# Kernel optimization log

Hardware: AMD Instinct MI355X
Metric: run time of the kernel (lower is better)

## Reference

```python
import jax, jax.numpy as jnp
import numpy as np

B, T, N, D, E, H = 4, 512, 512, 1024, 1024, 16
HD = D // H
EPS = 1e-6

def _ln(h):
    mu = jnp.mean(h, axis=-1, keepdims=True)
    var = jnp.mean(jnp.square(h - mu), axis=-1, keepdims=True)
    return (h - mu) / jnp.sqrt(var + EPS)

def setup_inputs() -> dict:
    key = jax.random.key(0)
    ks = jax.random.split(key, 20)
    s = 0.02
    return {
        "x1": jax.random.normal(ks[0], (B, T, D), jnp.float32),
        "x2": jax.random.normal(ks[1], (B, T, D), jnp.float32),
        "x3": jax.random.normal(ks[2], (B, T, D), jnp.float32),
        "xf": jax.random.normal(ks[3], (B, N, D), jnp.float32),
        "emb": jax.random.normal(ks[4], (B, E), jnp.float32),
        "key_padding_mask": jnp.zeros((B, N), dtype=bool),
        # AdaLN params (branch-stacked), weights stored (in,out)
        "adaln_w": jax.random.normal(ks[5], (3, E, 2 * D), jnp.float32) * s,
        "adaln_b": jnp.zeros((3, 2 * D), jnp.float32),
        "xf_adaln_w": jax.random.normal(ks[6], (E, 2 * D), jnp.float32) * s,
        "xf_adaln_b": jnp.zeros((2 * D,), jnp.float32),
        "q_w": jax.random.normal(ks[7], (3, D, D), jnp.float32) * s,
        "q_b": jnp.zeros((3, D), jnp.float32),
        "k_w": jax.random.normal(ks[8], (D, D), jnp.float32) * s,
        "k_b": jnp.zeros((D,), jnp.float32),
        "v_w": jax.random.normal(ks[9], (D, D), jnp.float32) * s,
        "v_b": jnp.zeros((D,), jnp.float32),
        "out_w": jax.random.normal(ks[10], (3, D, D), jnp.float32) * s,
        "out_b": jnp.zeros((3, D), jnp.float32),
    }

def reference(x1, x2, x3, xf, emb, key_padding_mask,
              adaln_w, adaln_b, xf_adaln_w, xf_adaln_b,
              q_w, q_b, k_w, k_b, v_w, v_b, out_w, out_b):
    se = jax.nn.silu(emb)  # (B,E)
    xs = [x1, x2, x3]
    Qs = []
    for i in range(3):
        eo = se @ adaln_w[i] + adaln_b[i]            # (B,2D)
        scale, shift = jnp.split(eo, 2, axis=-1)
        h = _ln(xs[i]) * (1.0 + scale[:, None]) + shift[:, None]
        Qs.append((h @ q_w[i] + q_b[i]).reshape(B, T, H, HD))
    Q = jnp.concatenate(Qs, axis=1)                  # (B,3T,H,HD)

    eo = se @ xf_adaln_w + xf_adaln_b
    scale, shift = jnp.split(eo, 2, axis=-1)
    xfn = _ln(xf) * (1.0 + scale[:, None]) + shift[:, None]
    K = (xfn @ k_w + k_b).reshape(B, N, H, HD)
    V = (xfn @ v_w + v_b).reshape(B, N, H, HD)

    logits = jnp.einsum('bthd,bnhd->bhtn', Q, K) / jnp.sqrt(jnp.float32(HD))
    logits = jnp.where(key_padding_mask[:, None, None, :], -jnp.inf, logits)
    attn = jax.nn.softmax(logits, axis=-1)           # dropout is identity (eval)
    out = jnp.einsum('bhtn,bnhd->bthd', attn, V).reshape(B, 3 * T, D)

    out1 = out[:, :T] @ out_w[0] + out_b[0]
    out2 = out[:, T:2 * T] @ out_w[1] + out_b[1]
    out3 = out[:, 2 * T:3 * T] @ out_w[2] + out_b[2]
    return (out1, out2, out3)
```

## Files before the change

### kernel.cpp

```cpp
#include <hip/hip_runtime.h>
#include <hip/hip_bf16.h>
#include <stdint.h>

#define BB 4
#define TSEQ 512
#define NSEQ 512
#define DD 1024
#define EE 1024
#define HH 16
#define HD 64

typedef __attribute__((ext_vector_type(8))) short bf16x8;
typedef __attribute__((ext_vector_type(4))) float f32x4;

__device__ __forceinline__ unsigned short f2bf(float f) {
    union { float f; uint32_t u; } v; v.f = f;
    uint32_t u = v.u;
    uint32_t r = (u + 0x7fffu + ((u >> 16) & 1u)) >> 16;
    return (unsigned short)r;
}

__device__ __forceinline__ uint32_t pkbf(float a, float b) {
    __hip_bfloat162 t = __float22bfloat162_rn(float2{a, b});
    return *(uint32_t*)&t;
}

#define GLD16(gp, lp)                                                          \
    __builtin_amdgcn_global_load_lds(                                          \
        (const __attribute__((address_space(1))) unsigned int*)(gp),           \
        (__attribute__((address_space(3))) unsigned int*)(lp), 16, 0, 0)

__global__ __launch_bounds__(256) void tw_all_kernel(
    const float* __restrict__ q_w, const float* __restrict__ k_w,
    const float* __restrict__ v_w, const float* __restrict__ out_w,
    unsigned short* __restrict__ qwt, unsigned short* __restrict__ kwt,
    unsigned short* __restrict__ vwt, unsigned short* __restrict__ owt)
{
    __shared__ __align__(16) unsigned short Ts[64 * 72];
    int k0 = blockIdx.x * 64, n0 = blockIdx.y * 64;
    int z = blockIdx.z;
    const float* in; unsigned short* out;
    if (z < 3)       { in = q_w + (size_t)z * DD * DD;         out = qwt + (size_t)z * DD * DD; }
    else if (z == 3) { in = k_w;                               out = kwt; }
    else if (z == 4) { in = v_w;                               out = vwt; }
    else             { in = out_w + (size_t)(z - 5) * DD * DD; out = owt + (size_t)(z - 5) * DD * DD; }
    int tid = threadIdx.x;
    int r = tid >> 2, c0 = (tid & 3) * 16;
#pragma unroll
    for (int i = 0; i < 4; i++) {
        float4 v = *(const float4*)(in + (size_t)(k0 + r) * DD + n0 + c0 + i * 4);
        Ts[(c0 + i * 4 + 0) * 72 + r] = f2bf(v.x);
        Ts[(c0 + i * 4 + 1) * 72 + r] = f2bf(v.y);
        Ts[(c0 + i * 4 + 2) * 72 + r] = f2bf(v.z);
        Ts[(c0 + i * 4 + 3) * 72 + r] = f2bf(v.w);
    }
    __syncthreads();
#pragma unroll
    for (int i = 0; i < 2; i++) {
        int idx = i * 256 + tid;
        int row = idx >> 3, ko = (idx & 7) * 8;
        *(uint4*)(out + (size_t)(n0 + row) * DD + k0 + ko) =
            *(const uint4*)(Ts + row * 72 + ko);
    }
}

__global__ __launch_bounds__(256) void adaln_kernel(
    const float* __restrict__ emb,
    const float* __restrict__ adaln_w, const float* __restrict__ adaln_b,
    const float* __restrict__ xf_w, const float* __restrict__ xf_b,
    float* __restrict__ scaleB, float* __restrict__ shiftB)
{
    __shared__ __align__(16) float seT[EE][4];
    __shared__ float buf[128 * 33];
    int tid = threadIdx.x;
    int chunk = blockIdx.x, j = blockIdx.y;
#pragma unroll
    for (int b = 0; b < 4; b++) {
        float4 e4 = ((const float4*)(emb + (size_t)b * EE))[tid];
        seT[tid * 4 + 0][b] = e4.x / (1.f + __expf(-e4.x));
        seT[tid * 4 + 1][b] = e4.y / (1.f + __expf(-e4.y));
        seT[tid * 4 + 2][b] = e4.z / (1.f + __expf(-e4.z));
        seT[tid * 4 + 3][b] = e4.w / (1.f + __expf(-e4.w));
    }
    __syncthreads();
    const float* W    = (j < 3) ? (adaln_w + (size_t)j * EE * 2 * DD) : xf_w;
    const float* bias = (j < 3) ? (adaln_b + (size_t)j * 2 * DD) : xf_b;
    int eg = tid >> 3, cg = tid & 7;
    int c0 = chunk * 32 + cg * 4;
    const float* Wp = W + (size_t)(eg * 32) * (2 * DD) + c0;
    float4 a0 = {0,0,0,0}, a1 = {0,0,0,0}, a2 = {0,0,0,0}, a3 = {0,0,0,0};
#pragma unroll 8
    for (int e = 0; e < 32; e++) {
        float4 w = *(const float4*)(Wp + (size_t)e * (2 * DD));
        float4 s = *(const float4*)&seT[eg * 32 + e][0];
        a0.x += s.x * w.x; a0.y += s.x * w.y; a0.z += s.x * w.z; a0.w += s.x * w.w;
        a1.x += s.y * w.x; a1.y += s.y * w.y; a1.z += s.y * w.z; a1.w += s.y * w.w;
        a2.x += s.z * w.x; a2.y += s.z * w.y; a2.z += s.z * w.z; a2.w += s.z * w.w;
        a3.x += s.w * w.x; a3.y += s.w * w.y; a3.z += s.w * w.z; a3.w += s.w * w.w;
    }
    float accs[4][4] = {{a0.x,a0.y,a0.z,a0.w},{a1.x,a1.y,a1.z,a1.w},
                        {a2.x,a2.y,a2.z,a2.w},{a3.x,a3.y,a3.z,a3.w}};
#pragma unroll
    for (int b = 0; b < 4; b++)
#pragma unroll
        for (int i = 0; i < 4; i++)
            buf[(b * 32 + cg * 4 + i) * 33 + eg] = accs[b][i];
    __syncthreads();
    if (tid < 128) {
        int b = tid >> 5, cl = tid & 31;
        float s = 0.f;
#pragma unroll 8
        for (int e = 0; e < 32; e++) s += buf[(b * 32 + cl) * 33 + e];
        int c = chunk * 32 + cl;
        float v = s + bias[c];
        if (c < DD) scaleB[(size_t)(j * 4 + b) * DD + c] = v;
        else        shiftB[(size_t)(j * 4 + b) * DD + (c - DD)] = v;
    }
}

__global__ __launch_bounds__(256) void ln_mod_kernel(
    const float* __restrict__ x1, const float* __restrict__ x2,
    const float* __restrict__ x3, const float* __restrict__ xf,
    const float* __restrict__ scaleB, const float* __restrict__ shiftB,
    unsigned short* __restrict__ hq, unsigned short* __restrict__ hx)
{
    __shared__ float rs[4], rq[4];
    int row = blockIdx.x, tid = threadIdx.x;
    const float* src; unsigned short* dst; int sb;
    if (row < 6144) {
        int b = row / 1536, t3 = row % 1536;
        int br = t3 >> 9, t = t3 & 511;
        const float* xs = (br == 0) ? x1 : ((br == 1) ? x2 : x3);
        src = xs + ((size_t)b * TSEQ + t) * DD;
        dst = hq + (size_t)row * DD;
        sb = br * 4 + b;
    } else {
        int idx = row - 6144;
        src = xf + (size_t)idx * DD;
        dst = hx + (size_t)idx * DD;
        sb = 12 + (idx >> 9);
    }
    float4 x = ((const float4*)src)[tid];
    float s = x.x + x.y + x.z + x.w;
    float q = x.x * x.x + x.y * x.y + x.z * x.z + x.w * x.w;
    for (int o = 1; o < 64; o <<= 1) { s += __shfl_xor(s, o, 64); q += __shfl_xor(q, o, 64); }
    int lane = tid & 63, wid = tid >> 6;
    if (lane == 0) { rs[wid] = s; rq[wid] = q; }
    __syncthreads();
    float S = rs[0] + rs[1] + rs[2] + rs[3];
    float Q = rq[0] + rq[1] + rq[2] + rq[3];
    float mu = S * (1.f / DD);
    float var = Q * (1.f / DD) - mu * mu;
    float rstd = rsqrtf(var + 1e-6f);
    float4 sc = ((const float4*)(scaleB + (size_t)sb * DD))[tid];
    float4 sh = ((const float4*)(shiftB + (size_t)sb * DD))[tid];
    ushort4 o;
    o.x = f2bf((x.x - mu) * rstd * (1.f + sc.x) + sh.x);
    o.y = f2bf((x.y - mu) * rstd * (1.f + sc.y) + sh.y);
    o.z = f2bf((x.z - mu) * rstd * (1.f + sc.z) + sh.z);
    o.w = f2bf((x.w - mu) * rstd * (1.f + sc.w) + sh.w);
    ((ushort4*)dst)[tid] = o;
}

__device__ __forceinline__ void gemm_core64x128(
    const unsigned short* __restrict__ A, const unsigned short* __restrict__ W,
    int m0, int n0, unsigned short* As, unsigned short* Bs,
    int tid, f32x4 acc[2][4])
{
    int lane = tid & 63, wid = tid >> 6;
    int fm = lane & 15, quad = lane >> 4;
    int wm = wid >> 1, wn = wid & 1;
    int sr = tid >> 3;
    int sc = tid & 7;
    int gko = (sc ^ (sr & 7)) * 8;
    const unsigned short* Ap = A + (size_t)(m0 + sr) * DD + gko;
    const unsigned short* Wp = W + (size_t)(n0 + sr) * DD + gko;
    unsigned short* la = As + tid * 8;
    unsigned short* lb = Bs + tid * 8;
    int f7 = fm & 7;
    for (int k0 = 0; k0 < DD; k0 += 64) {
#pragma unroll
        for (int i = 0; i < 2; i++)
            GLD16(Ap + (size_t)(32 * i) * DD + k0, la + i * 2048);
#pragma unroll
        for (int i = 0; i < 4; i++)
            GLD16(Wp + (size_t)(32 * i) * DD + k0, lb + i * 2048);
        __syncthreads();
#pragma unroll
        for (int kh = 0; kh < 2; kh++) {
            int sq = ((quad + 4 * kh) ^ f7) * 8;
            bf16x8 af[2], bfr[4];
#pragma unroll
            for (int mt = 0; mt < 2; mt++)
                af[mt] = *(const bf16x8*)(As + (wm * 32 + mt * 16 + fm) * 64 + sq);
#pragma unroll
            for (int nt = 0; nt < 4; nt++)
                bfr[nt] = *(const bf16x8*)(Bs + (wn * 64 + nt * 16 + fm) * 64 + sq);
#pragma unroll
            for (int mt = 0; mt < 2; mt++)
#pragma unroll
                for (int nt = 0; nt < 4; nt++)
                    acc[mt][nt] = __builtin_amdgcn_mfma_f32_16x16x32_bf16(af[mt], bfr[nt], acc[mt][nt], 0, 0, 0);
        }
        __syncthreads();
    }
}

__global__ __launch_bounds__(256) void q_gemm(
    const unsigned short* __restrict__ hq, const unsigned short* __restrict__ qwt,
    const float* __restrict__ q_b, unsigned short* __restrict__ Qpk)
{
    __shared__ __align__(16) unsigned short As[64 * 64];
    __shared__ __align__(16) unsigned short Bs[128 * 64];
    int id = blockIdx.x;
    int ty = id % 96, n0 = (id / 96) * 128;
    int m0 = ty * 64;
    int br = (m0 % 1536) >> 9;
    const unsigned short* W = qwt + (size_t)br * DD * DD;
    const float* bias = q_b + (size_t)br * DD;
    int tid = threadIdx.x, lane = tid & 63, wid = tid >> 6;
    int fm = lane & 15, quad = lane >> 4;
    int wm = wid >> 1, wn = wid & 1;
    f32x4 z = {0.f, 0.f, 0.f, 0.f};
    f32x4 acc[2][4];
#pragma unroll
    for (int mt = 0; mt < 2; mt++)
#pragma unroll
        for (int nt = 0; nt < 4; nt++) acc[mt][nt] = z;
    gemm_core64x128(hq, W, m0, n0, As, Bs, tid, acc);
#pragma unroll
    for (int mt = 0; mt < 2; mt++) {
#pragma unroll
        for (int nt = 0; nt < 4; nt++) {
            int c = n0 + wn * 64 + nt * 16 + fm;
            float bv = bias[c];
            int r0 = m0 + wm * 32 + mt * 16 + quad * 4;
            int h = c >> 6;
            int b = r0 / 1536, t3 = r0 % 1536;
            int kk = (c >> 5) & 1, o = c & 31;
            size_t base = ((((size_t)(b * HH + h) * 2 + kk) * 1536) + t3) * 32 + o;
#pragma unroll
            for (int reg = 0; reg < 4; reg++)
                Qpk[base + (size_t)reg * 32] = f2bf((acc[mt][nt][reg] + bv) * 0.125f);
        }
    }
}

__global__ __launch_bounds__(256) void kv_gemm(
    const unsigned short* __restrict__ hx,
    const unsigned short* __restrict__ kwt, const unsigned short* __restrict__ vwt,
    const float* __restrict__ k_b, const float* __restrict__ v_b,
    unsigned short* __restrict__ Kpk, unsigned short* __restrict__ Vpk)
{
    __shared__ __align__(16) unsigned short As[64 * 64];
    __shared__ __align__(16) unsigned short Bs[128 * 64];
    int id = blockIdx.x;
    int ty = id % 64, n0 = (id / 64) * 128;
    int isV = ty >> 5;
    int m0 = (ty & 31) * 64;
    const unsigned short* W = isV ? vwt : kwt;
    const float* bias = isV ? v_b : k_b;
    int tid = threadIdx.x, lane = tid & 63, wid = tid >> 6;
    int fm = lane & 15, quad = lane >> 4;
    int wm = wid >> 1, wn = wid & 1;
    f32x4 z = {0.f, 0.f, 0.f, 0.f};
    f32x4 acc[2][4];
#pragma unroll
    for (int mt = 0; mt < 2; mt++)
#pragma unroll
        for (int nt = 0; nt < 4; nt++) acc[mt][nt] = z;
    gemm_core64x128(hx, W, m0, n0, As, Bs, tid, acc);
#pragma unroll
    for (int mt = 0; mt < 2; mt++) {
#pragma unroll
        for (int nt = 0; nt < 4; nt++) {
            int c = n0 + wn * 64 + nt * 16 + fm;
            float bv = bias[c];
            int r0 = m0 + wm * 32 + mt * 16 + quad * 4;
            int h = c >> 6;
            int b = r0 >> 9, n = r0 & 511;
            if (!isV) {
                int kk = (c >> 5) & 1, o = c & 31;
                size_t base = ((((size_t)(b * HH + h) * 2 + kk) * 512) + n) * 32 + o;
#pragma unroll
                for (int reg = 0; reg < 4; reg++)
                    Kpk[base + (size_t)reg * 32] = f2bf(acc[mt][nt][reg] + bv);
            } else {
                int hd = c & 63, cv = n >> 5, ko = n & 31;
                ushort4 st;
                st.x = f2bf(acc[mt][nt][0] + bv);
                st.y = f2bf(acc[mt][nt][1] + bv);
                st.z = f2bf(acc[mt][nt][2] + bv);
                st.w = f2bf(acc[mt][nt][3] + bv);
                *(ushort4*)(Vpk + ((((size_t)(b * HH + h) * 16 + cv) * 64) + hd) * 32 + ko) = st;
            }
        }
    }
}

__global__ __launch_bounds__(256) void out_gemm(
    const unsigned short* __restrict__ Ain, const unsigned short* __restrict__ owt,
    const float* __restrict__ out_b, float* __restrict__ outp)
{
    __shared__ __align__(16) unsigned short As[64 * 64];
    __shared__ __align__(16) unsigned short Bs[128 * 64];
    int id = blockIdx.x;
    int ty = id % 96, n0 = (id / 96) * 128;
    int m0 = ty * 64;
    int br = (m0 % 1536) >> 9;
    const unsigned short* W = owt + (size_t)br * DD * DD;
    const float* bias = out_b + (size_t)br * DD;
    int tid = threadIdx.x, lane = tid & 63, wid = tid >> 6;
    int fm = lane & 15, quad = lane >> 4;
    int wm = wid >> 1, wn = wid & 1;
    f32x4 z = {0.f, 0.f, 0.f, 0.f};
    f32x4 acc[2][4];
#pragma unroll
    for (int mt = 0; mt < 2; mt++)
#pragma unroll
        for (int nt = 0; nt < 4; nt++) acc[mt][nt] = z;
    gemm_core64x128(Ain, W, m0, n0, As, Bs, tid, acc);
#pragma unroll
    for (int mt = 0; mt < 2; mt++) {
#pragma unroll
        for (int nt = 0; nt < 4; nt++) {
            int c = n0 + wn * 64 + nt * 16 + fm;
            float bv = bias[c];
            int r0 = m0 + wm * 32 + mt * 16 + quad * 4;
            int b = r0 / 1536, t3 = r0 % 1536, t = t3 & 511;
#pragma unroll
            for (int reg = 0; reg < 4; reg++)
                outp[(size_t)br * (BB * TSEQ * DD) + (size_t)b * (TSEQ * DD)
                     + (size_t)(t + reg) * DD + c] = acc[mt][nt][reg] + bv;
        }
    }
}

__global__ __launch_bounds__(256, 4) void attn_kernel(
    const unsigned short* __restrict__ Qpk,
    const unsigned short* __restrict__ Kpk,
    const unsigned short* __restrict__ Vpk,
    const unsigned char* __restrict__ mask,
    unsigned short* __restrict__ attn)
{
    __shared__ __align__(16) unsigned short P[32 * 520];
    __shared__ float redsum[128];
    int orig = blockIdx.x;
    int wg = (orig & 7) * 384 + (orig >> 3);
    int bh = wg / 48, b = bh >> 4, h = bh & 15;
    int m0 = (wg % 48) * 32;
    int tid = threadIdx.x, lane = tid & 63, w = tid >> 6;
    int fm = lane & 15, quad = lane >> 4;

    const unsigned char* mp = mask + (size_t)b * NSEQ + w * 128;
    unsigned long long mw0 = __ballot(mp[lane] != 0);
    unsigned long long mw1 = __ballot(mp[64 + lane] != 0);

    f32x4 acc[8][2];
#pragma unroll
    for (int mt = 0; mt < 8; mt++) {
        unsigned long long word = (mt >= 4) ? mw1 : mw0;
        int kb = (mt * 16 + quad * 4) & 63;
        f32x4 ini;
#pragma unroll
        for (int reg = 0; reg < 4; reg++)
            ini[reg] = ((word >> (kb + reg)) & 1ull) ? -1e30f : 0.f;
        acc[mt][0] = ini; acc[mt][1] = ini;
    }
    const unsigned short* Kbase = Kpk + (size_t)bh * 2 * 512 * 32 + quad * 8;
    const unsigned short* Qbase = Qpk + (size_t)bh * 2 * 1536 * 32 + quad * 8;
    const unsigned short* Vbase = Vpk + (size_t)bh * 16 * 64 * 32 + (size_t)(w * 16 + fm) * 32 + quad * 8;
#pragma unroll
    for (int kk = 0; kk < 2; kk++) {
        bf16x8 bq0 = *(const bf16x8*)(Qbase + (size_t)(kk * 1536 + m0 + fm) * 32);
        bf16x8 bq1 = *(const bf16x8*)(Qbase + (size_t)(kk * 1536 + m0 + 16 + fm) * 32);
#pragma unroll
        for (int mt = 0; mt < 8; mt++) {
            bf16x8 ak = *(const bf16x8*)(Kbase + (size_t)(kk * 512 + w * 128 + mt * 16 + fm) * 32);
            acc[mt][0] = __builtin_amdgcn_mfma_f32_16x16x32_bf16(ak, bq0, acc[mt][0], 0, 0, 0);
            acc[mt][1] = __builtin_amdgcn_mfma_f32_16x16x32_bf16(ak, bq1, acc[mt][1], 0, 0, 0);
        }
    }

    bf16x8 vpre[8];
#pragma unroll
    for (int kk = 0; kk < 8; kk++)
        vpre[kk] = *(const bf16x8*)(Vbase + (size_t)kk * 64 * 32);

    float s0 = 0.f, s1 = 0.f;
#pragma unroll
    for (int mt = 0; mt < 8; mt++) {
        float e00 = __expf(acc[mt][0][0]);
        float e01 = __expf(acc[mt][0][1]);
        float e02 = __expf(acc[mt][0][2]);
        float e03 = __expf(acc[mt][0][3]);
        float e10 = __expf(acc[mt][1][0]);
        float e11 = __expf(acc[mt][1][1]);
        float e12 = __expf(acc[mt][1][2]);
        float e13 = __expf(acc[mt][1][3]);
        s0 += (e00 + e01) + (e02 + e03);
        s1 += (e10 + e11) + (e12 + e13);
        uint2 p0, p1;
        p0.x = pkbf(e00, e01); p0.y = pkbf(e02, e03);
        p1.x = pkbf(e10, e11); p1.y = pkbf(e12, e13);
        int kb = w * 128 + mt * 16 + quad * 4;
        *(uint2*)(P + (size_t)fm * 520 + kb) = p0;
        *(uint2*)(P + (size_t)(16 + fm) * 520 + kb) = p1;
    }
    s0 += __shfl_xor(s0, 16, 64); s0 += __shfl_xor(s0, 32, 64);
    s1 += __shfl_xor(s1, 16, 64); s1 += __shfl_xor(s1, 32, 64);
    if (quad == 0) { redsum[w * 32 + fm] = s0; redsum[w * 32 + 16 + fm] = s1; }
    __syncthreads();

    float inv0 = 1.f / (redsum[fm] + redsum[32 + fm] + redsum[64 + fm] + redsum[96 + fm]);
    float inv1 = 1.f / (redsum[16 + fm] + redsum[48 + fm] + redsum[80 + fm] + redsum[112 + fm]);
    bf16x8 vrest[8];
#pragma unroll
    for (int kk = 0; kk < 8; kk++)
        vrest[kk] = *(const bf16x8*)(Vbase + (size_t)(8 + kk) * 64 * 32);
    f32x4 z = {0.f, 0.f, 0.f, 0.f};
    f32x4 o0 = z, o1 = z;
    const unsigned short* Pp0 = P + (size_t)fm * 520 + quad * 8;
    const unsigned short* Pp1 = P + (size_t)(16 + fm) * 520 + quad * 8;
#pragma unroll
    for (int kk = 0; kk < 8; kk++) {
        bf16x8 p0 = *(const bf16x8*)(Pp0 + kk * 32);
        bf16x8 p1 = *(const bf16x8*)(Pp1 + kk * 32);
        o0 = __builtin_amdgcn_mfma_f32_16x16x32_bf16(vpre[kk], p0, o0, 0, 0, 0);
        o1 = __builtin_amdgcn_mfma_f32_16x16x32_bf16(vpre[kk], p1, o1, 0, 0, 0);
    }
#pragma unroll
    for (int kk = 0; kk < 8; kk++) {
        bf16x8 p0 = *(const bf16x8*)(Pp0 + (8 + kk) * 32);
        bf16x8 p1 = *(const bf16x8*)(Pp1 + (8 + kk) * 32);
        o0 = __builtin_amdgcn_mfma_f32_16x16x32_bf16(vrest[kk], p0, o0, 0, 0, 0);
        o1 = __builtin_amdgcn_mfma_f32_16x16x32_bf16(vrest[kk], p1, o1, 0, 0, 0);
    }
    ushort4 r0, r1;
    r0.x = f2bf(o0[0] * inv0); r0.y = f2bf(o0[1] * inv0);
    r0.z = f2bf(o0[2] * inv0); r0.w = f2bf(o0[3] * inv0);
    r1.x = f2bf(o1[0] * inv1); r1.y = f2bf(o1[1] * inv1);
    r1.z = f2bf(o1[2] * inv1); r1.w = f2bf(o1[3] * inv1);
    *(ushort4*)(attn + ((size_t)(b * 1536 + m0 + fm)) * DD + h * HD + w * 16 + quad * 4) = r0;
    *(ushort4*)(attn + ((size_t)(b * 1536 + m0 + 16 + fm)) * DD + h * HD + w * 16 + quad * 4) = r1;
}

extern "C" void kernel_launch(void* const* d_in, const int* in_sizes, int n_in,
                              void* d_out, int out_size, void* d_ws, size_t ws_size,
                              hipStream_t stream)
{
    const float* x1   = (const float*)d_in[0];
    const float* x2   = (const float*)d_in[1];
    const float* x3   = (const float*)d_in[2];
    const float* xf   = (const float*)d_in[3];
    const float* emb  = (const float*)d_in[4];
    const unsigned char* mask = (const unsigned char*)d_in[5];
    const float* adaln_w = (const float*)d_in[6];
    const float* adaln_b = (const float*)d_in[7];
    const float* xf_w = (const float*)d_in[8];
    const float* xf_b = (const float*)d_in[9];
    const float* q_w  = (const float*)d_in[10];
    const float* q_b  = (const float*)d_in[11];
    const float* k_w  = (const float*)d_in[12];
    const float* k_b  = (const float*)d_in[13];
    const float* v_w  = (const float*)d_in[14];
    const float* v_b  = (const float*)d_in[15];
    const float* out_w = (const float*)d_in[16];
    const float* out_b = (const float*)d_in[17];

    char* ws = (char*)d_ws;
    float* scaleB        = (float*)(ws + 0);
    float* shiftB        = (float*)(ws + 65536);
    unsigned short* hq   = (unsigned short*)(ws + 131072);
    unsigned short* hx   = (unsigned short*)(ws + 12713984);
    unsigned short* Qpk  = (unsigned short*)(ws + 16908288);
    unsigned short* Kpk  = (unsigned short*)(ws + 29491200);
    unsigned short* Vpk  = (unsigned short*)(ws + 33685504);
    unsigned short* qwt  = (unsigned short*)(ws + 37879808);
    unsigned short* kwt  = (unsigned short*)(ws + 44171264);
    unsigned short* vwt  = (unsigned short*)(ws + 46268416);
    unsigned short* owt  = (unsigned short*)(ws + 48365568);

    tw_all_kernel<<<dim3(16, 16, 8), 256, 0, stream>>>(q_w, k_w, v_w, out_w,
                                                       qwt, kwt, vwt, owt);
    adaln_kernel<<<dim3(64, 4), 256, 0, stream>>>(emb, adaln_w, adaln_b, xf_w, xf_b,
                                                  scaleB, shiftB);
    ln_mod_kernel<<<8192, 256, 0, stream>>>(x1, x2, x3, xf, scaleB, shiftB, hq, hx);
    kv_gemm<<<512, 256, 0, stream>>>(hx, kwt, vwt, k_b, v_b, Kpk, Vpk);
    q_gemm<<<768, 256, 0, stream>>>(hq, qwt, q_b, Qpk);
    attn_kernel<<<3072, 256, 0, stream>>>(Qpk, Kpk, Vpk, mask, hq);
    out_gemm<<<768, 256, 0, stream>>>(hq, owt, out_b, (float*)d_out);
}
```

Measured before the change: 260.5 us.

## Halve attention query tile to 16 rows and double grid for occupancy

The attention kernel now processes 16 query rows per workgroup instead of 32. Grid size doubles to 6144 and the launch bound rises to 6 waves per SIMD. V fragments are no longer prefetched into registers but loaded inline in the PV loop, which cuts register and LDS use. The trade-off is that each K and V tile is reused by half as many query rows, so K/V traffic doubles, and the PV loop loses its prefetch overlap.

```diff
diff --git a/kernel.cpp b/kernel.cpp
--- a/kernel.cpp
+++ b/kernel.cpp
@@ -336,19 +336,19 @@
     }
 }
 
-__global__ __launch_bounds__(256, 4) void attn_kernel(
+__global__ __launch_bounds__(256, 6) void attn_kernel(
     const unsigned short* __restrict__ Qpk,
     const unsigned short* __restrict__ Kpk,
     const unsigned short* __restrict__ Vpk,
     const unsigned char* __restrict__ mask,
     unsigned short* __restrict__ attn)
 {
-    __shared__ __align__(16) unsigned short P[32 * 520];
-    __shared__ float redsum[128];
+    __shared__ __align__(16) unsigned short P[16 * 520];
+    __shared__ float redsum[64];
     int orig = blockIdx.x;
-    int wg = (orig & 7) * 384 + (orig >> 3);
-    int bh = wg / 48, b = bh >> 4, h = bh & 15;
-    int m0 = (wg % 48) * 32;
+    int wg = (orig & 7) * 768 + (orig >> 3);
+    int bh = wg / 96, b = bh >> 4, h = bh & 15;
+    int m0 = (wg % 96) * 16;
     int tid = threadIdx.x, lane = tid & 63, w = tid >> 6;
     int fm = lane & 15, quad = lane >> 4;
 
@@ -356,7 +356,7 @@
     unsigned long long mw0 = __ballot(mp[lane] != 0);
     unsigned long long mw1 = __ballot(mp[64 + lane] != 0);
 
-    f32x4 acc[8][2];
+    f32x4 acc[8];
 #pragma unroll
     for (int mt = 0; mt < 8; mt++) {
         unsigned long long word = (mt >= 4) ? mw1 : mw0;
@@ -365,84 +365,52 @@
 #pragma unroll
         for (int reg = 0; reg < 4; reg++)
             ini[reg] = ((word >> (kb + reg)) & 1ull) ? -1e30f : 0.f;
-        acc[mt][0] = ini; acc[mt][1] = ini;
+        acc[mt] = ini;
     }
     const unsigned short* Kbase = Kpk + (size_t)bh * 2 * 512 * 32 + quad * 8;
     const unsigned short* Qbase = Qpk + (size_t)bh * 2 * 1536 * 32 + quad * 8;
     const unsigned short* Vbase = Vpk + (size_t)bh * 16 * 64 * 32 + (size_t)(w * 16 + fm) * 32 + quad * 8;
 #pragma unroll
     for (int kk = 0; kk < 2; kk++) {
-        bf16x8 bq0 = *(const bf16x8*)(Qbase + (size_t)(kk * 1536 + m0 + fm) * 32);
-        bf16x8 bq1 = *(const bf16x8*)(Qbase + (size_t)(kk * 1536 + m0 + 16 + fm) * 32);
+        bf16x8 bq = *(const bf16x8*)(Qbase + (size_t)(kk * 1536 + m0 + fm) * 32);
 #pragma unroll
         for (int mt = 0; mt < 8; mt++) {
             bf16x8 ak = *(const bf16x8*)(Kbase + (size_t)(kk * 512 + w * 128 + mt * 16 + fm) * 32);
-            acc[mt][0] = __builtin_amdgcn_mfma_f32_16x16x32_bf16(ak, bq0, acc[mt][0], 0, 0, 0);
-            acc[mt][1] = __builtin_amdgcn_mfma_f32_16x16x32_bf16(ak, bq1, acc[mt][1], 0, 0, 0);
+            acc[mt] = __builtin_amdgcn_mfma_f32_16x16x32_bf16(ak, bq, acc[mt], 0, 0, 0);
         }
     }
 
-    bf16x8 vpre[8];
-#pragma unroll
-    for (int kk = 0; kk < 8; kk++)
-        vpre[kk] = *(const bf16x8*)(Vbase + (size_t)kk * 64 * 32);
-
-    float s0 = 0.f, s1 = 0.f;
+    float s0 = 0.f;
 #pragma unroll
     for (int mt = 0; mt < 8; mt++) {
-        float e00 = __expf(acc[mt][0][0]);
-        float e01 = __expf(acc[mt][0][1]);
-        float e02 = __expf(acc[mt][0][2]);
-        float e03 = __expf(acc[mt][0][3]);
-        float e10 = __expf(acc[mt][1][0]);
-        float e11 = __expf(acc[mt][1][1]);
-        float e12 = __expf(acc[mt][1][2]);
-        float e13 = __expf(acc[mt][1][3]);
-        s0 += (e00 + e01) + (e02 + e03);
-        s1 += (e10 + e11) + (e12 + e13);
-        uint2 p0, p1;
-        p0.x = pkbf(e00, e01); p0.y = pkbf(e02, e03);
-        p1.x = pkbf(e10, e11); p1.y = pkbf(e12, e13);
+        float e0 = __expf(acc[mt][0]);
+        float e1 = __expf(acc[mt][1]);
+        float e2 = __expf(acc[mt][2]);
+        float e3 = __expf(acc[mt][3]);
+        s0 += (e0 + e1) + (e2 + e3);
+        uint2 p;
+        p.x = pkbf(e0, e1); p.y = pkbf(e2, e3);
         int kb = w * 128 + mt * 16 + quad * 4;
-        *(uint2*)(P + (size_t)fm * 520 + kb) = p0;
-        *(uint2*)(P + (size_t)(16 + fm) * 520 + kb) = p1;
-    }
-    s0 += __shfl_xor(s0, 16, 64); s0 += __shfl_xor(s0, 32, 64);
-    s1 += __shfl_xor(s1, 16, 64); s1 += __shfl_xor(s1, 32, 64);
-    if (quad == 0) { redsum[w * 32 + fm] = s0; redsum[w * 32 + 16 + fm] = s1; }
+        *(uint2*)(P + (size_t)fm * 520 + kb) = p;
+    }
+    s0 += __shfl_xor(s0, 16, 64);
+    s0 += __shfl_xor(s0, 32, 64);
+    if (quad == 0) redsum[w * 16 + fm] = s0;
     __syncthreads();
 
-    float inv0 = 1.f / (redsum[fm] + redsum[32 + fm] + redsum[64 + fm] + redsum[96 + fm]);
-    float inv1 = 1.f / (redsum[16 + fm] + redsum[48 + fm] + redsum[80 + fm] + redsum[112 + fm]);
-    bf16x8 vrest[8];
-#pragma unroll
-    for (int kk = 0; kk < 8; kk++)
-        vrest[kk] = *(const bf16x8*)(Vbase + (size_t)(8 + kk) * 64 * 32);
-    f32x4 z = {0.f, 0.f, 0.f, 0.f};
-    f32x4 o0 = z, o1 = z;
+    float inv0 = 1.f / (redsum[fm] + redsum[16 + fm] + redsum[32 + fm] + redsum[48 + fm]);
+    f32x4 o0 = {0.f, 0.f, 0.f, 0.f};
     const unsigned short* Pp0 = P + (size_t)fm * 520 + quad * 8;
-    const unsigned short* Pp1 = P + (size_t)(16 + fm) * 520 + quad * 8;
-#pragma unroll
-    for (int kk = 0; kk < 8; kk++) {
+#pragma unroll
+    for (int kk = 0; kk < 16; kk++) {
+        bf16x8 av = *(const bf16x8*)(Vbase + (size_t)kk * 64 * 32);
         bf16x8 p0 = *(const bf16x8*)(Pp0 + kk * 32);
-        bf16x8 p1 = *(const bf16x8*)(Pp1 + kk * 32);
-        o0 = __builtin_amdgcn_mfma_f32_16x16x32_bf16(vpre[kk], p0, o0, 0, 0, 0);
-        o1 = __builtin_amdgcn_mfma_f32_16x16x32_bf16(vpre[kk], p1, o1, 0, 0, 0);
-    }
-#pragma unroll
-    for (int kk = 0; kk < 8; kk++) {
-        bf16x8 p0 = *(const bf16x8*)(Pp0 + (8 + kk) * 32);
-        bf16x8 p1 = *(const bf16x8*)(Pp1 + (8 + kk) * 32);
-        o0 = __builtin_amdgcn_mfma_f32_16x16x32_bf16(vrest[kk], p0, o0, 0, 0, 0);
-        o1 = __builtin_amdgcn_mfma_f32_16x16x32_bf16(vrest[kk], p1, o1, 0, 0, 0);
-    }
-    ushort4 r0, r1;
+        o0 = __builtin_amdgcn_mfma_f32_16x16x32_bf16(av, p0, o0, 0, 0, 0);
+    }
+    ushort4 r0;
     r0.x = f2bf(o0[0] * inv0); r0.y = f2bf(o0[1] * inv0);
     r0.z = f2bf(o0[2] * inv0); r0.w = f2bf(o0[3] * inv0);
-    r1.x = f2bf(o1[0] * inv1); r1.y = f2bf(o1[1] * inv1);
-    r1.z = f2bf(o1[2] * inv1); r1.w = f2bf(o1[3] * inv1);
     *(ushort4*)(attn + ((size_t)(b * 1536 + m0 + fm)) * DD + h * HD + w * 16 + quad * 4) = r0;
-    *(ushort4*)(attn + ((size_t)(b * 1536 + m0 + 16 + fm)) * DD + h * HD + w * 16 + quad * 4) = r1;
 }
 
 extern "C" void kernel_launch(void* const* d_in, const int* in_sizes, int n_in,
@@ -488,6 +456,6 @@
     ln_mod_kernel<<<8192, 256, 0, stream>>>(x1, x2, x3, xf, scaleB, shiftB, hq, hx);
     kv_gemm<<<512, 256, 0, stream>>>(hx, kwt, vwt, k_b, v_b, Kpk, Vpk);
     q_gemm<<<768, 256, 0, stream>>>(hq, qwt, q_b, Qpk);
-    attn_kernel<<<3072, 256, 0, stream>>>(Qpk, Kpk, Vpk, mask, hq);
+    attn_kernel<<<6144, 256, 0, stream>>>(Qpk, Kpk, Vpk, mask, hq);
     out_gemm<<<768, 256, 0, stream>>>(hq, owt, out_b, (float*)d_out);
 }
```

Result: slower. 274.9 us (+5.5%).
